# Performance work log

Measured on AMD Instinct MI355X. Metric: run time of the kernel, lower is better.

Reference implementation:

```python
import jax, jax.numpy as jnp
import numpy as np

C_IN, C_OUT, G = 64, 64, 32
D_MODEL = C_IN + 4 * G            # 192
DI = 2 * D_MODEL                  # d_inner = 384 (expand=2)
N_STATE = 16
DT_RANK = (D_MODEL + 15) // 16    # 12
K_DIR = 4
B, H, W = 2, 64, 64


def setup_inputs() -> dict:
    key = jax.random.key(0)
    ks = jax.random.split(key, 16)
    rn = lambda k, shp, s=0.02: jax.random.normal(k, shp, jnp.float32) * s
    inp = {"x": jax.random.normal(ks[0], (B, C_IN, H, W), jnp.float32)}
    chans = [C_IN, C_IN + G, C_IN + 2 * G, C_IN + 3 * G]
    for i, ci in enumerate(chans):
        inp[f"c{i+1}_w"] = rn(ks[1 + i], (G, ci, 3, 3))
        inp[f"c{i+1}_b"] = jnp.zeros((G,), jnp.float32)
    inp["c5_w"] = rn(ks[5], (C_OUT, D_MODEL, 3, 3))
    inp["c5_b"] = jnp.zeros((C_OUT,), jnp.float32)
    inp["ln1_g"] = jnp.ones((D_MODEL,), jnp.float32)
    inp["ln1_b"] = jnp.zeros((D_MODEL,), jnp.float32)
    inp["in_proj_w"] = rn(ks[6], (2 * DI, D_MODEL))
    inp["dw_w"] = rn(ks[7], (DI, 1, 3, 3))          # depthwise conv kernel
    inp["dw_b"] = jnp.zeros((DI,), jnp.float32)
    inp["x_proj_w"] = rn(ks[8], (K_DIR, DT_RANK + 2 * N_STATE, DI))
    inp["dt_w"] = rn(ks[9], (K_DIR, DI, DT_RANK), 0.1)
    inp["dt_b"] = jax.random.uniform(ks[10], (K_DIR, DI), jnp.float32, -4.0, -2.0)
    inp["A_logs"] = jnp.log(jnp.tile(jnp.arange(1, N_STATE + 1, dtype=jnp.float32), (K_DIR, DI, 1)))
    inp["Ds"] = jnp.ones((K_DIR, DI), jnp.float32)
    inp["out_norm_g"] = jnp.ones((DI,), jnp.float32)
    inp["out_norm_b"] = jnp.zeros((DI,), jnp.float32)
    inp["out_proj_w"] = rn(ks[11], (D_MODEL, DI))
    return inp


def conv2d(x, w, b, groups=1):
    y = jax.lax.conv_general_dilated(x, w, (1, 1), 'SAME',
                                     feature_group_count=groups,
                                     dimension_numbers=('NCHW', 'OIHW', 'NCHW'))
    return y + b[None, :, None, None]


def layer_norm(x, g, b, eps=1e-5):
    mu = jnp.mean(x, -1, keepdims=True)
    var = jnp.var(x, -1, keepdims=True)
    return (x - mu) * jax.lax.rsqrt(var + eps) * g + b


def selective_scan(u, delta, A, Bm, Cm, D):
    # u, delta: (B,K,Dm,L); Bm, Cm: (B,K,N,L); A: (K,Dm,N); D: (K,Dm)
    uL = jnp.moveaxis(u, -1, 0)
    dL = jnp.moveaxis(delta, -1, 0)
    BL = jnp.moveaxis(Bm, -1, 0)
    CL = jnp.moveaxis(Cm, -1, 0)
    h0 = jnp.zeros(u.shape[:3] + (A.shape[-1],), u.dtype)  # (B,K,Dm,N)

    def step(h, inp):
        u_l, d_l, B_l, C_l = inp
        dA = jnp.exp(d_l[..., None] * A)                              # (B,K,Dm,N)
        h = dA * h + (d_l * u_l)[..., None] * B_l[:, :, None, :]
        y = jnp.einsum('bkdn,bkn->bkd', h, C_l)
        return h, y

    _, ys = jax.lax.scan(step, h0, (uL, dL, BL, CL))
    y = jnp.moveaxis(ys, 0, -1)                                       # (B,K,Dm,L)
    return y + D[None, :, :, None] * u


def vss_block(x, ln1_g, ln1_b, in_proj_w, dw_w, dw_b, x_proj_w, dt_w, dt_b,
              A_logs, Ds, out_norm_g, out_norm_b, out_proj_w):
    Bn, C, Hh, Ww = x.shape
    L = Hh * Ww
    di = in_proj_w.shape[0] // 2
    nst = A_logs.shape[-1]
    dtr = dt_w.shape[-1]
    xi = jnp.transpose(x, (0, 2, 3, 1))                               # BHWC
    xn = layer_norm(xi, ln1_g, ln1_b)
    xz = xn @ in_proj_w.T                                             # (B,H,W,2*di)
    xp, z = jnp.split(xz, 2, -1)
    xc = jnp.transpose(xp, (0, 3, 1, 2))                              # (B,di,H,W)
    xc = jax.nn.silu(conv2d(xc, dw_w, dw_b, groups=di))
    xf = xc.reshape(Bn, di, L)
    xt = jnp.transpose(xc, (0, 1, 3, 2)).reshape(Bn, di, L)
    xs = jnp.stack([xf, xt, xf[..., ::-1], xt[..., ::-1]], 1)         # (B,4,di,L)
    x_dbl = jnp.einsum('bkdl,kcd->bkcl', xs, x_proj_w)
    dts = jnp.einsum('bkrl,kdr->bkdl', x_dbl[:, :, :dtr], dt_w)
    Bs = x_dbl[:, :, dtr:dtr + nst]
    Cs = x_dbl[:, :, dtr + nst:]
    delta = jax.nn.softplus(dts + dt_b[None, :, :, None])
    A = -jnp.exp(A_logs)
    oy = selective_scan(xs, delta, A, Bs, Cs, Ds)                     # (B,4,di,L)
    inv = oy[:, 2:4, :, ::-1]
    wh = jnp.transpose(oy[:, 1].reshape(Bn, di, Ww, Hh), (0, 1, 3, 2)).reshape(Bn, di, L)
    iwh = jnp.transpose(inv[:, 1].reshape(Bn, di, Ww, Hh), (0, 1, 3, 2)).reshape(Bn, di, L)
    y = oy[:, 0] + inv[:, 0] + wh + iwh
    y = jnp.transpose(y, (0, 2, 1)).reshape(Bn, Hh, Ww, di)
    y = layer_norm(y, out_norm_g, out_norm_b)
    y = y * jax.nn.silu(z)
    out = xi + y @ out_proj_w.T                                       # residual (VSSBlock)
    return jnp.transpose(out, (0, 3, 1, 2))


def reference(x, c1_w, c1_b, c2_w, c2_b, c3_w, c3_b, c4_w, c4_b, c5_w, c5_b,
              ln1_g, ln1_b, in_proj_w, dw_w, dw_b, x_proj_w, dt_w, dt_b,
              A_logs, Ds, out_norm_g, out_norm_b, out_proj_w):
    lrelu = lambda t: jax.nn.leaky_relu(t, 0.01)
    x1 = lrelu(conv2d(x, c1_w, c1_b))
    x2 = lrelu(conv2d(jnp.concatenate([x, x1], 1), c2_w, c2_b))
    x3 = lrelu(conv2d(jnp.concatenate([x, x1, x2], 1), c3_w, c3_b))
    x4 = lrelu(conv2d(jnp.concatenate([x, x1, x2, x3], 1), c4_w, c4_b))
    f = jnp.concatenate([x, x1, x2, x3, x4], 1)                       # (B,192,H,W)
    sa = vss_block(f, ln1_g, ln1_b, in_proj_w, dw_w, dw_b, x_proj_w, dt_w, dt_b,
                   A_logs, Ds, out_norm_g, out_norm_b, out_proj_w)
    return conv2d(sa, c5_w, c5_b)
```

## Files before the change

### kernel.cpp

```cpp
#include <hip/hip_runtime.h>
#include <hip/hip_bf16.h>
#include <math.h>

static constexpr int LEN = 4096;
static constexpr int HN  = 64;
static constexpr int WN  = 64;
static constexpr int NB  = 2;
static constexpr int DM  = 192;
static constexpr int DIM = 384;
static constexpr int NST = 16;
static constexpr int DTR = 12;
static constexpr int KD  = 4;
static constexpr int NC  = 64;
static constexpr int CHL = LEN / NC;

typedef __attribute__((ext_vector_type(8))) short bfrag;
typedef __attribute__((ext_vector_type(4))) float facc;

__device__ __forceinline__ unsigned short f2bf(float x) {
    unsigned int u = __float_as_uint(x);
    return (unsigned short)((u + 0x7FFFu + ((u >> 16) & 1u)) >> 16);
}

__device__ __forceinline__ int maprow(int k, int gl) {
    int g = (k & 2) ? (LEN - 1 - gl) : gl;
    return (k & 1) ? (((g & 63) << 6) | (g >> 6)) : g;
}

__global__ void k_wtr(const float* __restrict__ w, float* __restrict__ wt,
                      int cin, int cout, int n)
{
    int idx = blockIdx.x * 256 + threadIdx.x;
    if (idx >= n) return;
    int ci = idx % cin; int r = idx / cin;
    int co = r % cout; int t = r / cout;
    wt[idx] = w[((size_t)(co * cin + ci)) * 9 + t];
}

__global__ void k_wxp(const float* __restrict__ xpw, float* __restrict__ WX)
{
    int idx = blockIdx.x * 256 + threadIdx.x;
    if (idx >= 192 * DIM) return;
    int row = idx / DIM, d = idx - row * DIM;
    int k = row / 48, c = row - k * 48;
    WX[idx] = (c < 44) ? xpw[((size_t)(k * 44 + c)) * DIM + d] : 0.f;
}

__global__ void k_tr_in(const float* __restrict__ x, float* __restrict__ FN)
{
    __shared__ float t[64][65];
    int b = blockIdx.y, r = blockIdx.x;
    int tid = threadIdx.x;
#pragma unroll
    for (int i = 0; i < 16; ++i) {
        int idx = (i << 8) + tid;
        int c = idx >> 6, xc = idx & 63;
        t[c][xc] = x[((size_t)(b * 64 + c)) * LEN + r * WN + xc];
    }
    __syncthreads();
#pragma unroll
    for (int i = 0; i < 16; ++i) {
        int idx = (i << 8) + tid;
        int px = idx >> 6, c = idx & 63;
        FN[((size_t)(b * LEN + r * WN + px)) * DM + c] = t[c][px];
    }
}

__global__ void __launch_bounds__(256) k_convmf(
    const float* __restrict__ in, int cbuf, int cin, int cout,
    const float* __restrict__ wt2,
    float* __restrict__ part)
{
    __shared__ unsigned short Asb[66][40];
    __shared__ unsigned short Bsb[3][32][40];
    int zz = blockIdx.z;
    int b = zz / 3, s = zz % 3;
    int y0 = blockIdx.x;
    int n0 = blockIdx.y << 5;
    int tid = threadIdx.x;
    int wv = tid >> 6, lane = tid & 63;
    int mb  = (wv & 1) << 5;
    int nbw = (wv >> 1) << 4;
    int lr = lane & 15, lq = lane >> 4;
    int y = y0 + s - 1;
    bool yok = (unsigned)y < (unsigned)HN;
    const float* inb = in + ((size_t)b * LEN + (size_t)y * WN) * cbuf;

    facc acc0 = (facc){0,0,0,0}, acc1 = (facc){0,0,0,0};

    for (int ci0 = 0; ci0 < cin; ci0 += 32) {
#pragma unroll
        for (int it = 0; it < 3; ++it) {
            int fi = (it << 8) + tid;
            if (fi < 528) {
                int px = fi >> 3, c4 = (fi & 7) << 2;
                int xx = px - 1;
                float4 v = make_float4(0.f, 0.f, 0.f, 0.f);
                if (yok && (unsigned)xx < (unsigned)WN)
                    v = *(const float4*)(inb + (size_t)xx * cbuf + ci0 + c4);
                ushort4 u; u.x = f2bf(v.x); u.y = f2bf(v.y); u.z = f2bf(v.z); u.w = f2bf(v.w);
                *(ushort4*)(&Asb[px][c4]) = u;
            }
        }
#pragma unroll
        for (int it = 0; it < 3; ++it) {
            int fi = (it << 8) + tid;
            int dx = fi >> 8; int rem = fi & 255;
            int oc = rem >> 3, c4 = (rem & 7) << 2;
            int t = s * 3 + dx;
            float4 v = *(const float4*)(wt2 + ((size_t)(t * cout + n0 + oc)) * cin + ci0 + c4);
            ushort4 u; u.x = f2bf(v.x); u.y = f2bf(v.y); u.z = f2bf(v.z); u.w = f2bf(v.w);
            *(ushort4*)(&Bsb[dx][oc][c4]) = u;
        }
        __syncthreads();
#pragma unroll
        for (int dx = 0; dx < 3; ++dx) {
            bfrag a0 = *(const bfrag*)(&Asb[mb + lr + dx][lq * 8]);
            bfrag a1 = *(const bfrag*)(&Asb[mb + 16 + lr + dx][lq * 8]);
            bfrag b0 = *(const bfrag*)(&Bsb[dx][nbw + lr][lq * 8]);
            acc0 = __builtin_amdgcn_mfma_f32_16x16x32_bf16(a0, b0, acc0, 0, 0, 0);
            acc1 = __builtin_amdgcn_mfma_f32_16x16x32_bf16(a1, b0, acc1, 0, 0, 0);
        }
        __syncthreads();
    }
    float* pb = part + (((size_t)(s * NB + b) * LEN) + y0 * WN) * cout + n0 + nbw + lr;
#pragma unroll
    for (int r = 0; r < 4; ++r) {
        int px0 = mb + lq * 4 + r;
        pb[(size_t)px0 * cout] = acc0[r];
        pb[(size_t)(px0 + 16) * cout] = acc1[r];
    }
}

__global__ void k_ep_nhwc(const float* __restrict__ part, const float* __restrict__ bias,
                          float* __restrict__ FN, int co0, float slope)
{
    int idx = blockIdx.x * 256 + threadIdx.x;
    int co = idx & 31, px = idx >> 5;
    const size_t S = (size_t)NB * LEN * 32;
    float v = part[idx] + part[S + idx] + part[2 * S + idx] + bias[co];
    v = v > 0.f ? v : v * slope;
    FN[(size_t)px * DM + co0 + co] = v;
}

__global__ void k_ep_pl_tr(const float* __restrict__ part, const float* __restrict__ bias,
                           float* __restrict__ out)
{
    __shared__ float t[64][65];
    int b = blockIdx.y, l0 = blockIdx.x << 6;
    int tid = threadIdx.x;
    const size_t S = (size_t)NB * LEN * 64;
#pragma unroll
    for (int i = 0; i < 16; ++i) {
        int idx = (i << 8) + tid;
        int px = idx >> 6, oc = idx & 63;
        size_t o = ((size_t)b * LEN + l0 + px) * 64 + oc;
        t[px][oc] = part[o] + part[S + o] + part[2 * S + o] + bias[oc];
    }
    __syncthreads();
#pragma unroll
    for (int i = 0; i < 16; ++i) {
        int idx = (i << 8) + tid;
        int oc = idx >> 6, px = idx & 63;
        out[((size_t)(b * 64 + oc)) * LEN + l0 + px] = t[px][oc];
    }
}

__global__ void k_lnstat(const float* __restrict__ FN, float* __restrict__ MU,
                         float* __restrict__ RS)
{
    int lane = threadIdx.x & 63;
    int pix  = (blockIdx.x << 2) + (threadIdx.x >> 6);
    const float* fp = FN + (size_t)pix * DM;
    float v0 = fp[lane];
    float v1 = fp[lane + 64];
    float v2 = fp[lane + 128];
    float s = v0 + v1 + v2, ss = v0 * v0 + v1 * v1 + v2 * v2;
#pragma unroll
    for (int off = 1; off < 64; off <<= 1) { s += __shfl_xor(s, off); ss += __shfl_xor(ss, off); }
    if (lane == 0) {
        float mu = s * (1.f / 192.f);
        float var = ss * (1.f / 192.f) - mu * mu;
        MU[pix] = mu;
        RS[pix] = rsqrtf(var + 1e-5f);
    }
}

struct MfTile { facc a00, a01, a10, a11; int mb, nb, lr, lq; };

__device__ __forceinline__ MfTile mf_gemm_core(
    const float* __restrict__ A, int K, const float* __restrict__ Wt,
    int b, int l0, int n0, unsigned short (*Asb)[72], unsigned short (*Bsb)[72])
{
    int tid = threadIdx.x;
    MfTile t;
    t.a00 = (facc){0,0,0,0}; t.a01 = (facc){0,0,0,0};
    t.a10 = (facc){0,0,0,0}; t.a11 = (facc){0,0,0,0};
    int wv = tid >> 6, lane = tid & 63;
    t.mb = (wv & 1) << 5; t.nb = (wv >> 1) << 5;
    t.lr = lane & 15; t.lq = lane >> 4;

    for (int k0 = 0; k0 < K; k0 += 64) {
#pragma unroll
        for (int s = 0; s < 4; ++s) {
            int idx = (s << 8) + tid;
            int row = idx >> 4, c4 = (idx & 15) << 2;
            float4 av = *(const float4*)(A + ((size_t)b * LEN + l0 + row) * K + k0 + c4);
            ushort4 ua; ua.x = f2bf(av.x); ua.y = f2bf(av.y); ua.z = f2bf(av.z); ua.w = f2bf(av.w);
            *(ushort4*)(&Asb[row][c4]) = ua;
            float4 wvv = *(const float4*)(Wt + (size_t)(n0 + row) * K + k0 + c4);
            ushort4 ub; ub.x = f2bf(wvv.x); ub.y = f2bf(wvv.y); ub.z = f2bf(wvv.z); ub.w = f2bf(wvv.w);
            *(ushort4*)(&Bsb[row][c4]) = ub;
        }
        __syncthreads();
#pragma unroll
        for (int kk = 0; kk < 64; kk += 32) {
            bfrag a0 = *(const bfrag*)(&Asb[t.mb + t.lr][kk + t.lq * 8]);
            bfrag a1 = *(const bfrag*)(&Asb[t.mb + 16 + t.lr][kk + t.lq * 8]);
            bfrag b0 = *(const bfrag*)(&Bsb[t.nb + t.lr][kk + t.lq * 8]);
            bfrag b1 = *(const bfrag*)(&Bsb[t.nb + 16 + t.lr][kk + t.lq * 8]);
            t.a00 = __builtin_amdgcn_mfma_f32_16x16x32_bf16(a0, b0, t.a00, 0, 0, 0);
            t.a01 = __builtin_amdgcn_mfma_f32_16x16x32_bf16(a0, b1, t.a01, 0, 0, 0);
            t.a10 = __builtin_amdgcn_mfma_f32_16x16x32_bf16(a1, b0, t.a10, 0, 0, 0);
            t.a11 = __builtin_amdgcn_mfma_f32_16x16x32_bf16(a1, b1, t.a11, 0, 0, 0);
        }
        __syncthreads();
    }
    return t;
}

__device__ __forceinline__ void mf_store(
    facc v, float* __restrict__ Cp, const float* __restrict__ res,
    int b, int l0, int n0, int outC, int lr, int lq)
{
#pragma unroll
    for (int r = 0; r < 4; ++r) {
        int m = lq * 4 + r, n = lr;
        size_t o = ((size_t)b * LEN + l0 + m) * outC + n0 + n;
        float x = v[r];
        if (res) x += res[o];
        Cp[o] = x;
    }
}

__global__ void __launch_bounds__(256) k_gemm_mf(
    const float* __restrict__ A, int K, const float* __restrict__ Wt,
    const float* __restrict__ res, float* __restrict__ Cp, int outC)
{
    __shared__ unsigned short Asb[64][72];
    __shared__ unsigned short Bsb[64][72];
    int b = blockIdx.z, l0 = blockIdx.x << 6, n0 = blockIdx.y << 6;
    MfTile t = mf_gemm_core(A, K, Wt, b, l0, n0, Asb, Bsb);
    mf_store(t.a00, Cp, res, b, l0 + t.mb,      n0 + t.nb,      outC, t.lr, t.lq);
    mf_store(t.a01, Cp, res, b, l0 + t.mb,      n0 + t.nb + 16, outC, t.lr, t.lq);
    mf_store(t.a10, Cp, res, b, l0 + t.mb + 16, n0 + t.nb,      outC, t.lr, t.lq);
    mf_store(t.a11, Cp, res, b, l0 + t.mb + 16, n0 + t.nb + 16, outC, t.lr, t.lq);
}

__global__ void __launch_bounds__(256) k_gemm_ipmf(
    const float* __restrict__ A, const float* __restrict__ Wt,
    const float* __restrict__ g, const float* __restrict__ be,
    const float* __restrict__ MU, const float* __restrict__ RS,
    float* __restrict__ XPN, float* __restrict__ ZT)
{
    __shared__ unsigned short Asb[64][72];
    __shared__ unsigned short Bsb[64][72];
    int b = blockIdx.z, l0 = blockIdx.x << 6, n0 = blockIdx.y << 6;
    int tid = threadIdx.x;
    MfTile t;
    t.a00 = (facc){0,0,0,0}; t.a01 = (facc){0,0,0,0};
    t.a10 = (facc){0,0,0,0}; t.a11 = (facc){0,0,0,0};
    int wv = tid >> 6, lane = tid & 63;
    t.mb = (wv & 1) << 5; t.nb = (wv >> 1) << 5;
    t.lr = lane & 15; t.lq = lane >> 4;

    for (int k0 = 0; k0 < DM; k0 += 64) {
#pragma unroll
        for (int s = 0; s < 4; ++s) {
            int idx = (s << 8) + tid;
            int row = idx >> 4, c4 = (idx & 15) << 2;
            size_t pix = (size_t)b * LEN + l0 + row;
            float4 av = *(const float4*)(A + pix * DM + k0 + c4);
            float mu = MU[pix], rs = RS[pix];
            float4 gv = *(const float4*)(g + k0 + c4);
            float4 bv = *(const float4*)(be + k0 + c4);
            av.x = (av.x - mu) * rs * gv.x + bv.x;
            av.y = (av.y - mu) * rs * gv.y + bv.y;
            av.z = (av.z - mu) * rs * gv.z + bv.z;
            av.w = (av.w - mu) * rs * gv.w + bv.w;
            ushort4 ua; ua.x = f2bf(av.x); ua.y = f2bf(av.y); ua.z = f2bf(av.z); ua.w = f2bf(av.w);
            *(ushort4*)(&Asb[row][c4]) = ua;
            float4 wvv = *(const float4*)(Wt + (size_t)(n0 + row) * DM + k0 + c4);
            ushort4 ub; ub.x = f2bf(wvv.x); ub.y = f2bf(wvv.y); ub.z = f2bf(wvv.z); ub.w = f2bf(wvv.w);
            *(ushort4*)(&Bsb[row][c4]) = ub;
        }
        __syncthreads();
#pragma unroll
        for (int kk = 0; kk < 64; kk += 32) {
            bfrag a0 = *(const bfrag*)(&Asb[t.mb + t.lr][kk + t.lq * 8]);
            bfrag a1 = *(const bfrag*)(&Asb[t.mb + 16 + t.lr][kk + t.lq * 8]);
            bfrag b0 = *(const bfrag*)(&Bsb[t.nb + t.lr][kk + t.lq * 8]);
            bfrag b1 = *(const bfrag*)(&Bsb[t.nb + 16 + t.lr][kk + t.lq * 8]);
            t.a00 = __builtin_amdgcn_mfma_f32_16x16x32_bf16(a0, b0, t.a00, 0, 0, 0);
            t.a01 = __builtin_amdgcn_mfma_f32_16x16x32_bf16(a0, b1, t.a01, 0, 0, 0);
            t.a10 = __builtin_amdgcn_mfma_f32_16x16x32_bf16(a1, b0, t.a10, 0, 0, 0);
            t.a11 = __builtin_amdgcn_mfma_f32_16x16x32_bf16(a1, b1, t.a11, 0, 0, 0);
        }
        __syncthreads();
    }
    float* out = (blockIdx.y < 6) ? XPN : ZT;
    int nc = (blockIdx.y < 6) ? n0 : n0 - DIM;
    mf_store(t.a00, out, nullptr, b, l0 + t.mb,      nc + t.nb,      DIM, t.lr, t.lq);
    mf_store(t.a01, out, nullptr, b, l0 + t.mb,      nc + t.nb + 16, DIM, t.lr, t.lq);
    mf_store(t.a10, out, nullptr, b, l0 + t.mb + 16, nc + t.nb,      DIM, t.lr, t.lq);
    mf_store(t.a11, out, nullptr, b, l0 + t.mb + 16, nc + t.nb + 16, DIM, t.lr, t.lq);
}

__global__ void __launch_bounds__(256) k_dw(
    const float* __restrict__ xpn, const float* __restrict__ w,
    const float* __restrict__ bias, float* __restrict__ unh)
{
    int b = blockIdx.z, cg = blockIdx.y, r = blockIdx.x;
    int lane = threadIdx.x & 63, wv = threadIdx.x >> 6;
    int c = cg * 64 + lane;
    float wl[9];
#pragma unroll
    for (int t = 0; t < 9; ++t) wl[t] = w[c * 9 + t];
    float bv = bias[c];
    const float* base = xpn + (size_t)b * LEN * DIM + c;
    float* ob = unh + (size_t)b * LEN * DIM + c;
#pragma unroll 4
    for (int xi = 0; xi < 16; ++xi) {
        int x = wv * 16 + xi;
        float acc = bv;
#pragma unroll
        for (int dy = 0; dy < 3; ++dy) {
            int ry = r + dy - 1;
            if ((unsigned)ry >= (unsigned)HN) continue;
#pragma unroll
            for (int dx = 0; dx < 3; ++dx) {
                int xx = x + dx - 1;
                if ((unsigned)xx >= (unsigned)WN) continue;
                acc += base[(size_t)(ry * WN + xx) * DIM] * wl[dy * 3 + dx];
            }
        }
        acc = acc / (1.f + __expf(-acc));
        ob[(size_t)(r * WN + x) * DIM] = acc;
    }
}

__global__ void __launch_bounds__(384) k_delta(
    const float* __restrict__ CX, const float* __restrict__ dtw,
    const float* __restrict__ dtb, float* __restrict__ dlt)
{
    __shared__ float cs[16][12];
    int b = blockIdx.z, k = blockIdx.y;
    int lp0 = blockIdx.x << 4;
    int tid = threadIdx.x;
    if (tid < 192) {
        int p = tid / 12, r = tid - p * 12;
        cs[p][r] = CX[((size_t)(b * LEN) + lp0 + p) * 192 + k * 48 + r];
    }
    __syncthreads();
    float wt[DTR];
    const float* wp = dtw + ((size_t)(k * DIM) + tid) * DTR;
#pragma unroll
    for (int r = 0; r < DTR; ++r) wt[r] = wp[r];
    float bv = dtb[k * DIM + tid];
    float* dbase = dlt + (((size_t)(b * LEN) + lp0) * KD + k) * DIM + tid;
#pragma unroll
    for (int p = 0; p < 16; ++p) {
        float s = bv;
#pragma unroll
        for (int r = 0; r < DTR; ++r) s += cs[p][r] * wt[r];
        s = (s > 20.f) ? s : __logf(1.f + __expf(s));
        dbase[(size_t)p * KD * DIM] = s;
    }
}

__global__ void __launch_bounds__(384) k_scan_a(
    const float* __restrict__ unh, const float* __restrict__ CX,
    const float* __restrict__ alog, const float* __restrict__ dlt,
    float* __restrict__ hf, float* __restrict__ pA)
{
    __shared__ float bs[CHL * 16];
    int b = blockIdx.z, k = blockIdx.y, c = blockIdx.x;
    int d = threadIdx.x;
    for (int i = threadIdx.x; i < CHL * 16; i += 384) {
        int l = i >> 4, n = i & 15;
        int row = maprow(k, c * CHL + l);
        bs[i] = CX[((size_t)(b * LEN) + row) * 192 + k * 48 + 12 + n];
    }
    __syncthreads();

    float A[16], h[16];
    const float* ap = alog + ((size_t)(k * DIM + d)) * NST;
#pragma unroll
    for (int q = 0; q < 4; ++q) {
        float4 av = *(const float4*)(ap + q * 4);
        A[q * 4]     = -__expf(av.x); A[q * 4 + 1] = -__expf(av.y);
        A[q * 4 + 2] = -__expf(av.z); A[q * 4 + 3] = -__expf(av.w);
    }
    bool geo = true;
#pragma unroll
    for (int n = 1; n < 16; ++n)
        geo = geo && (fabsf(A[n] - (n + 1) * A[0]) <= 1e-4f * (n + 1) * fabsf(A[0]));
#pragma unroll
    for (int n = 0; n < 16; ++n) h[n] = 0.f;

    const float* ub = unh + (size_t)b * LEN * DIM + d;
    const float* db = dlt + ((size_t)(b * LEN) * KD + k) * DIM + d;
    size_t base = (((size_t)((b * KD + k) * NC + c)) * NST) * DIM + d;

    float dvA[4], uuA[4], dvB[4], uuB[4], dvC[4], uuC[4];
#pragma unroll
    for (int j = 0; j < 4; ++j) {
        int row = maprow(k, c * CHL + j);
        dvA[j] = db[(size_t)row * KD * DIM];
        uuA[j] = ub[(size_t)row * DIM];
    }
#pragma unroll
    for (int j = 0; j < 4; ++j) {
        int row = maprow(k, c * CHL + 4 + j);
        dvB[j] = db[(size_t)row * KD * DIM];
        uuB[j] = ub[(size_t)row * DIM];
    }

    if (geo) {
        float A0 = A[0];
        float p0 = 1.f;
        for (int l0 = 0; l0 < CHL; l0 += 4) {
            if (l0 + 8 < CHL) {
#pragma unroll
                for (int j = 0; j < 4; ++j) {
                    int row = maprow(k, c * CHL + l0 + 8 + j);
                    dvC[j] = db[(size_t)row * KD * DIM];
                    uuC[j] = ub[(size_t)row * DIM];
                }
            }
            __builtin_amdgcn_s_setprio(1);
#pragma unroll
            for (int j = 0; j < 4; ++j) {
                float du = dvA[j] * uuA[j];
                const float* bl = bs + (l0 + j) * 16;
                float qv = __expf(dvA[j] * A0);
                float pw = qv;
                h[0] = qv * h[0] + du * bl[0];
#pragma unroll
                for (int n = 1; n < 16; ++n) { pw *= qv; h[n] = pw * h[n] + du * bl[n]; }
                p0 *= qv;
            }
            __builtin_amdgcn_s_setprio(0);
#pragma unroll
            for (int j = 0; j < 4; ++j) { dvA[j] = dvB[j]; uuA[j] = uuB[j]; dvB[j] = dvC[j]; uuB[j] = uuC[j]; }
        }
        float pw = 1.f;
#pragma unroll
        for (int n = 0; n < 16; ++n) {
            pw *= p0;
            hf[base + (size_t)n * DIM] = h[n];
            pA[base + (size_t)n * DIM] = pw;
        }
    } else {
        float p[16];
#pragma unroll
        for (int n = 0; n < 16; ++n) p[n] = 1.f;
        for (int l0 = 0; l0 < CHL; l0 += 4) {
            if (l0 + 8 < CHL) {
#pragma unroll
                for (int j = 0; j < 4; ++j) {
                    int row = maprow(k, c * CHL + l0 + 8 + j);
                    dvC[j] = db[(size_t)row * KD * DIM];
                    uuC[j] = ub[(size_t)row * DIM];
                }
            }
#pragma unroll
            for (int j = 0; j < 4; ++j) {
                float du = dvA[j] * uuA[j];
                const float* bl = bs + (l0 + j) * 16;
#pragma unroll
                for (int n = 0; n < 16; ++n) {
                    float dA = __expf(dvA[j] * A[n]);
                    h[n] = dA * h[n] + du * bl[n];
                    p[n] *= dA;
                }
            }
#pragma unroll
            for (int j = 0; j < 4; ++j) { dvA[j] = dvB[j]; uuA[j] = uuB[j]; dvB[j] = dvC[j]; uuB[j] = uuC[j]; }
        }
#pragma unroll
        for (int n = 0; n < 16; ++n) {
            hf[base + (size_t)n * DIM] = h[n];
            pA[base + (size_t)n * DIM] = p[n];
        }
    }
}

__global__ void k_scan_b(float* __restrict__ hf, const float* __restrict__ pA)
{
    int s = blockIdx.x * 256 + threadIdx.x;
    int bk = s / (NST * DIM);
    int r  = s - bk * (NST * DIM);
    size_t base = (size_t)bk * NC * NST * DIM + r;
    const size_t cs = (size_t)NST * DIM;
    float car = 0.f;
#pragma unroll 8
    for (int c = 0; c < NC; ++c) {
        float hfc = hf[base + c * cs], pc = pA[base + c * cs];
        hf[base + c * cs] = car;
        car = pc * car + hfc;
    }
}

__global__ void __launch_bounds__(384) k_scan_c(
    const float* __restrict__ unh, const float* __restrict__ CX,
    const float* __restrict__ alog, const float* __restrict__ hf,
    float* __restrict__ dlt)
{
    __shared__ float bs[CHL * 32];
    int b = blockIdx.z, k = blockIdx.y, c = blockIdx.x;
    int d = threadIdx.x;
    for (int i = threadIdx.x; i < CHL * 32; i += 384) {
        int l = i >> 5, n = i & 31;
        int row = maprow(k, c * CHL + l);
        bs[i] = CX[((size_t)(b * LEN) + row) * 192 + k * 48 + 12 + n];
    }
    __syncthreads();

    float A[16], h[16];
    const float* ap = alog + ((size_t)(k * DIM + d)) * NST;
#pragma unroll
    for (int q = 0; q < 4; ++q) {
        float4 av = *(const float4*)(ap + q * 4);
        A[q * 4]     = -__expf(av.x); A[q * 4 + 1] = -__expf(av.y);
        A[q * 4 + 2] = -__expf(av.z); A[q * 4 + 3] = -__expf(av.w);
    }
    bool geo = true;
#pragma unroll
    for (int n = 1; n < 16; ++n)
        geo = geo && (fabsf(A[n] - (n + 1) * A[0]) <= 1e-4f * (n + 1) * fabsf(A[0]));
    size_t base = (((size_t)((b * KD + k) * NC + c)) * NST) * DIM + d;
#pragma unroll
    for (int n = 0; n < 16; ++n) h[n] = hf[base + (size_t)n * DIM];

    const float* ub = unh + (size_t)b * LEN * DIM + d;
    float* db = dlt + ((size_t)(b * LEN) * KD + k) * DIM + d;

    int rowsA[4], rowsB[4], rowsC[4];
    float dvA[4], uuA[4], dvB[4], uuB[4], dvC[4], uuC[4];
#pragma unroll
    for (int j = 0; j < 4; ++j) {
        rowsA[j] = maprow(k, c * CHL + j);
        dvA[j] = db[(size_t)rowsA[j] * KD * DIM];
        uuA[j] = ub[(size_t)rowsA[j] * DIM];
    }
#pragma unroll
    for (int j = 0; j < 4; ++j) {
        rowsB[j] = maprow(k, c * CHL + 4 + j);
        dvB[j] = db[(size_t)rowsB[j] * KD * DIM];
        uuB[j] = ub[(size_t)rowsB[j] * DIM];
    }

    if (geo) {
        float A0 = A[0];
        for (int l0 = 0; l0 < CHL; l0 += 4) {
            if (l0 + 8 < CHL) {
#pragma unroll
                for (int j = 0; j < 4; ++j) {
                    rowsC[j] = maprow(k, c * CHL + l0 + 8 + j);
                    dvC[j] = db[(size_t)rowsC[j] * KD * DIM];
                    uuC[j] = ub[(size_t)rowsC[j] * DIM];
                }
            }
            float ys[4];
            __builtin_amdgcn_s_setprio(1);
#pragma unroll
            for (int j = 0; j < 4; ++j) {
                const float* bl = bs + (l0 + j) * 32;
                float du = dvA[j] * uuA[j];
                float qv = __expf(dvA[j] * A0);
                float pw = qv;
                h[0] = qv * h[0] + du * bl[0];
                float y = h[0] * bl[16];
#pragma unroll
                for (int n = 1; n < 16; ++n) {
                    pw *= qv;
                    h[n] = pw * h[n] + du * bl[n];
                    y += h[n] * bl[16 + n];
                }
                ys[j] = y;
            }
            __builtin_amdgcn_s_setprio(0);
#pragma unroll
            for (int j = 0; j < 4; ++j) db[(size_t)rowsA[j] * KD * DIM] = ys[j];
#pragma unroll
            for (int j = 0; j < 4; ++j) {
                rowsA[j] = rowsB[j]; dvA[j] = dvB[j]; uuA[j] = uuB[j];
                rowsB[j] = rowsC[j]; dvB[j] = dvC[j]; uuB[j] = uuC[j];
            }
        }
    } else {
        for (int l0 = 0; l0 < CHL; l0 += 4) {
            if (l0 + 8 < CHL) {
#pragma unroll
                for (int j = 0; j < 4; ++j) {
                    rowsC[j] = maprow(k, c * CHL + l0 + 8 + j);
                    dvC[j] = db[(size_t)rowsC[j] * KD * DIM];
                    uuC[j] = ub[(size_t)rowsC[j] * DIM];
                }
            }
            float ys[4];
#pragma unroll
            for (int j = 0; j < 4; ++j) {
                const float* bl = bs + (l0 + j) * 32;
                float du = dvA[j] * uuA[j];
                float y = 0.f;
#pragma unroll
                for (int n = 0; n < 16; ++n) {
                    float dA = __expf(dvA[j] * A[n]);
                    h[n] = dA * h[n] + du * bl[n];
                    y += h[n] * bl[16 + n];
                }
                ys[j] = y;
            }
#pragma unroll
            for (int j = 0; j < 4; ++j) db[(size_t)rowsA[j] * KD * DIM] = ys[j];
#pragma unroll
            for (int j = 0; j < 4; ++j) {
                rowsA[j] = rowsB[j]; dvA[j] = dvB[j]; uuA[j] = uuB[j];
                rowsB[j] = rowsC[j]; dvB[j] = dvC[j]; uuB[j] = uuC[j];
            }
        }
    }
}

__global__ void k_merge(const float* __restrict__ y4, const float* __restrict__ unh,
                        const float* __restrict__ Ds, const float* __restrict__ ong,
                        const float* __restrict__ onb, const float* __restrict__ zt,
                        float* __restrict__ yg)
{
    int lane = threadIdx.x & 63;
    int pix = (blockIdx.x << 2) + (threadIdx.x >> 6);
    const float* yp = y4 + (size_t)pix * KD * DIM;
    const float* up = unh + (size_t)pix * DIM;
    float v[6]; float s = 0.f, ss = 0.f;
#pragma unroll
    for (int j = 0; j < 6; ++j) {
        int d = lane + (j << 6);
        float y = yp[d] + yp[DIM + d] + yp[2 * DIM + d] + yp[3 * DIM + d];
        float dsum = Ds[d] + Ds[DIM + d] + Ds[2 * DIM + d] + Ds[3 * DIM + d];
        y += dsum * up[d];
        v[j] = y; s += y; ss += y * y;
    }
#pragma unroll
    for (int off = 1; off < 64; off <<= 1) { s += __shfl_xor(s, off); ss += __shfl_xor(ss, off); }
    float mu = s * (1.f / 384.f);
    float var = ss * (1.f / 384.f) - mu * mu;
    float rstd = rsqrtf(var + 1e-5f);
    const float* zp = zt + (size_t)pix * DIM;
    float* op = yg + (size_t)pix * DIM;
#pragma unroll
    for (int j = 0; j < 6; ++j) {
        int d = lane + (j << 6);
        float zz = zp[d];
        float gate = zz / (1.f + __expf(-zz));
        op[d] = ((v[j] - mu) * rstd * ong[d] + onb[d]) * gate;
    }
}

extern "C" void kernel_launch(void* const* d_in, const int* in_sizes, int n_in,
                              void* d_out, int out_size, void* d_ws, size_t ws_size,
                              hipStream_t stream)
{
    const float* x    = (const float*)d_in[0];
    const float* c1w  = (const float*)d_in[1];  const float* c1b = (const float*)d_in[2];
    const float* c2w  = (const float*)d_in[3];  const float* c2b = (const float*)d_in[4];
    const float* c3w  = (const float*)d_in[5];  const float* c3b = (const float*)d_in[6];
    const float* c4w  = (const float*)d_in[7];  const float* c4b = (const float*)d_in[8];
    const float* c5w  = (const float*)d_in[9];  const float* c5b = (const float*)d_in[10];
    const float* ln1g = (const float*)d_in[11]; const float* ln1b= (const float*)d_in[12];
    const float* ipw  = (const float*)d_in[13];
    const float* dww  = (const float*)d_in[14]; const float* dwb = (const float*)d_in[15];
    const float* xpw  = (const float*)d_in[16];
    const float* dtw  = (const float*)d_in[17]; const float* dtb = (const float*)d_in[18];
    const float* alog = (const float*)d_in[19]; const float* dsv = (const float*)d_in[20];
    const float* ong  = (const float*)d_in[21]; const float* onb = (const float*)d_in[22];
    const float* opw  = (const float*)d_in[23];
    float* out = (float*)d_out;

    float* ws   = (float*)d_ws;
    float* FN   = ws;
    float* XN   = FN   + 1572864;
    float* XPN  = XN   + 1572864;
    float* ZT   = XPN  + 3145728;
    float* XCNH = ZT   + 3145728;
    float* DLT  = XCNH + 3145728;
    float* HF   = DLT  + 12582912;
    float* WT14 = HF   + 3145728;
    float* WT5  = WT14 + 129024;
    float* WX   = WT5  + 110592;
    float* MU   = WX   + 73728;
    float* RS   = MU   + 8192;
    float* PA = XPN;
    float* CX = XN;
    float* PART = XN;
    float* YN = DLT;

    k_wtr<<<dim3(72),  256, 0, stream>>>(c1w, WT14,          64, 32, 9 * 64 * 32);
    k_wtr<<<dim3(108), 256, 0, stream>>>(c2w, WT14 + 18432,  96, 32, 9 * 96 * 32);
    k_wtr<<<dim3(144), 256, 0, stream>>>(c3w, WT14 + 46080, 128, 32, 9 * 128 * 32);
    k_wtr<<<dim3(180), 256, 0, stream>>>(c4w, WT14 + 82944, 160, 32, 9 * 160 * 32);
    k_wtr<<<dim3(432), 256, 0, stream>>>(c5w, WT5,          192, 64, 9 * 192 * 64);
    k_wxp<<<dim3(288), 256, 0, stream>>>(xpw, WX);

    k_tr_in<<<dim3(HN, NB), 256, 0, stream>>>(x, FN);
    k_convmf<<<dim3(64, 1, NB * 3), 256, 0, stream>>>(FN, DM, 64, 32, WT14, PART);
    k_ep_nhwc<<<dim3(1024), 256, 0, stream>>>(PART, c1b, FN, 64, 0.01f);
    k_convmf<<<dim3(64, 1, NB * 3), 256, 0, stream>>>(FN, DM, 96, 32, WT14 + 18432, PART);
    k_ep_nhwc<<<dim3(1024), 256, 0, stream>>>(PART, c2b, FN, 96, 0.01f);
    k_convmf<<<dim3(64, 1, NB * 3), 256, 0, stream>>>(FN, DM, 128, 32, WT14 + 46080, PART);
    k_ep_nhwc<<<dim3(1024), 256, 0, stream>>>(PART, c3b, FN, 128, 0.01f);
    k_convmf<<<dim3(64, 1, NB * 3), 256, 0, stream>>>(FN, DM, 160, 32, WT14 + 82944, PART);
    k_ep_nhwc<<<dim3(1024), 256, 0, stream>>>(PART, c4b, FN, 160, 0.01f);

    k_lnstat<<<dim3(NB * LEN / 4), 256, 0, stream>>>(FN, MU, RS);
    k_gemm_ipmf<<<dim3(LEN / 64, 12, NB), 256, 0, stream>>>(FN, ipw, ln1g, ln1b, MU, RS, XPN, ZT);
    k_dw<<<dim3(HN, DIM / 64, NB), 256, 0, stream>>>(XPN, dww, dwb, XCNH);
    k_gemm_mf<<<dim3(LEN / 64, 3, NB), 256, 0, stream>>>(XCNH, DIM, WX, nullptr, CX, 192);
    k_delta<<<dim3(LEN / 16, KD, NB), 384, 0, stream>>>(CX, dtw, dtb, DLT);
    k_scan_a<<<dim3(NC, KD, NB), 384, 0, stream>>>(XCNH, CX, alog, DLT, HF, PA);
    k_scan_b<<<dim3(NB * KD * NST * DIM / 256), 256, 0, stream>>>(HF, PA);
    k_scan_c<<<dim3(NC, KD, NB), 384, 0, stream>>>(XCNH, CX, alog, HF, DLT);
    k_merge<<<dim3(NB * LEN / 4), 256, 0, stream>>>(DLT, XCNH, dsv, ong, onb, ZT, XCNH);
    k_gemm_mf<<<dim3(LEN / 64, 3, NB), 256, 0, stream>>>(XCNH, DIM, opw, FN, YN, DM);

    k_convmf<<<dim3(64, 2, NB * 3), 256, 0, stream>>>(YN, DM, 192, 64, WT5, PART);
    k_ep_pl_tr<<<dim3(64, NB), 256, 0, stream>>>(PART, c5b, out);
}
```

Measured before the change: 297.5 us.

## Split scan state dimension across two half-wavefronts to double thread parallelism

Both chunked selective-scan kernels now launch 768 threads per block, with each channel's 16 state entries split between two half-wavefronts of 8. The geometric power chain is shortened by computing powers up to p8 and scaling the upper half by p8. The output y is combined with a cross-half shuffle, and the geometric-check flag is shared the same way. This cuts the serial per-thread work and register pressure so more waves can hide latency. In exchange, each lane loads delta and u redundantly, shuffles are added, and half the lanes sit idle on the store.

```diff
diff --git a/kernel.cpp b/kernel.cpp
--- a/kernel.cpp
+++ b/kernel.cpp
@@ -378,35 +378,44 @@
     }
 }
 
-__global__ void __launch_bounds__(384) k_scan_a(
+__global__ void __launch_bounds__(768) k_scan_a(
     const float* __restrict__ unh, const float* __restrict__ CX,
     const float* __restrict__ alog, const float* __restrict__ dlt,
     float* __restrict__ hf, float* __restrict__ pA)
 {
     __shared__ float bs[CHL * 16];
     int b = blockIdx.z, k = blockIdx.y, c = blockIdx.x;
-    int d = threadIdx.x;
-    for (int i = threadIdx.x; i < CHL * 16; i += 384) {
+    int tid = threadIdx.x;
+    int lane = tid & 63;
+    int d = ((tid >> 6) << 5) + (lane & 31);
+    int half = lane >> 5;
+    int nh = half << 3;
+
+    for (int i = tid; i < CHL * 16; i += 768) {
         int l = i >> 4, n = i & 15;
         int row = maprow(k, c * CHL + l);
         bs[i] = CX[((size_t)(b * LEN) + row) * 192 + k * 48 + 12 + n];
     }
     __syncthreads();
 
-    float A[16], h[16];
+    float A[8], h[8];
     const float* ap = alog + ((size_t)(k * DIM + d)) * NST;
-#pragma unroll
-    for (int q = 0; q < 4; ++q) {
-        float4 av = *(const float4*)(ap + q * 4);
+    float A0 = -__expf(ap[0]);
+#pragma unroll
+    for (int q = 0; q < 2; ++q) {
+        float4 av = *(const float4*)(ap + nh + q * 4);
         A[q * 4]     = -__expf(av.x); A[q * 4 + 1] = -__expf(av.y);
         A[q * 4 + 2] = -__expf(av.z); A[q * 4 + 3] = -__expf(av.w);
     }
     bool geo = true;
 #pragma unroll
-    for (int n = 1; n < 16; ++n)
-        geo = geo && (fabsf(A[n] - (n + 1) * A[0]) <= 1e-4f * (n + 1) * fabsf(A[0]));
-#pragma unroll
-    for (int n = 0; n < 16; ++n) h[n] = 0.f;
+    for (int i = 0; i < 8; ++i) {
+        int n = nh + i;
+        geo = geo && (fabsf(A[i] - (n + 1) * A0) <= 1e-4f * (n + 1) * fabsf(A0));
+    }
+    geo = geo && (bool)__shfl_xor((int)geo, 32);
+#pragma unroll
+    for (int i = 0; i < 8; ++i) h[i] = 0.f;
 
     const float* ub = unh + (size_t)b * LEN * DIM + d;
     const float* db = dlt + ((size_t)(b * LEN) * KD + k) * DIM + d;
@@ -427,7 +436,6 @@
     }
 
     if (geo) {
-        float A0 = A[0];
         float p0 = 1.f;
         for (int l0 = 0; l0 < CHL; l0 += 4) {
             if (l0 + 8 < CHL) {
@@ -442,29 +450,38 @@
 #pragma unroll
             for (int j = 0; j < 4; ++j) {
                 float du = dvA[j] * uuA[j];
-                const float* bl = bs + (l0 + j) * 16;
+                const float* bl = bs + (l0 + j) * 16 + nh;
                 float qv = __expf(dvA[j] * A0);
-                float pw = qv;
-                h[0] = qv * h[0] + du * bl[0];
-#pragma unroll
-                for (int n = 1; n < 16; ++n) { pw *= qv; h[n] = pw * h[n] + du * bl[n]; }
+                float p2 = qv * qv, p3 = p2 * qv, p4 = p2 * p2;
+                float p5 = p4 * qv, p6 = p4 * p2, p7 = p4 * p3, p8 = p4 * p4;
+                float m = half ? p8 : 1.f;
+                h[0] = (qv * m) * h[0] + du * bl[0];
+                h[1] = (p2 * m) * h[1] + du * bl[1];
+                h[2] = (p3 * m) * h[2] + du * bl[2];
+                h[3] = (p4 * m) * h[3] + du * bl[3];
+                h[4] = (p5 * m) * h[4] + du * bl[4];
+                h[5] = (p6 * m) * h[5] + du * bl[5];
+                h[6] = (p7 * m) * h[6] + du * bl[6];
+                h[7] = (p8 * m) * h[7] + du * bl[7];
                 p0 *= qv;
             }
             __builtin_amdgcn_s_setprio(0);
 #pragma unroll
             for (int j = 0; j < 4; ++j) { dvA[j] = dvB[j]; uuA[j] = uuB[j]; dvB[j] = dvC[j]; uuB[j] = uuC[j]; }
         }
-        float pw = 1.f;
-#pragma unroll
-        for (int n = 0; n < 16; ++n) {
-            pw *= p0;
-            hf[base + (size_t)n * DIM] = h[n];
-            pA[base + (size_t)n * DIM] = pw;
+        float q2 = p0 * p0, q3 = q2 * p0, q4 = q2 * q2;
+        float q5 = q4 * p0, q6 = q4 * q2, q7 = q4 * q3, q8 = q4 * q4;
+        float m0 = half ? q8 : 1.f;
+        float Pw[8] = {p0 * m0, q2 * m0, q3 * m0, q4 * m0, q5 * m0, q6 * m0, q7 * m0, q8 * m0};
+#pragma unroll
+        for (int i = 0; i < 8; ++i) {
+            hf[base + (size_t)(nh + i) * DIM] = h[i];
+            pA[base + (size_t)(nh + i) * DIM] = Pw[i];
         }
     } else {
-        float p[16];
-#pragma unroll
-        for (int n = 0; n < 16; ++n) p[n] = 1.f;
+        float p[8];
+#pragma unroll
+        for (int i = 0; i < 8; ++i) p[i] = 1.f;
         for (int l0 = 0; l0 < CHL; l0 += 4) {
             if (l0 + 8 < CHL) {
 #pragma unroll
@@ -477,21 +494,21 @@
 #pragma unroll
             for (int j = 0; j < 4; ++j) {
                 float du = dvA[j] * uuA[j];
-                const float* bl = bs + (l0 + j) * 16;
-#pragma unroll
-                for (int n = 0; n < 16; ++n) {
-                    float dA = __expf(dvA[j] * A[n]);
-                    h[n] = dA * h[n] + du * bl[n];
-                    p[n] *= dA;
+                const float* bl = bs + (l0 + j) * 16 + nh;
+#pragma unroll
+                for (int i = 0; i < 8; ++i) {
+                    float dA = __expf(dvA[j] * A[i]);
+                    h[i] = dA * h[i] + du * bl[i];
+                    p[i] *= dA;
                 }
             }
 #pragma unroll
             for (int j = 0; j < 4; ++j) { dvA[j] = dvB[j]; uuA[j] = uuB[j]; dvB[j] = dvC[j]; uuB[j] = uuC[j]; }
         }
 #pragma unroll
-        for (int n = 0; n < 16; ++n) {
-            hf[base + (size_t)n * DIM] = h[n];
-            pA[base + (size_t)n * DIM] = p[n];
+        for (int i = 0; i < 8; ++i) {
+            hf[base + (size_t)(nh + i) * DIM] = h[i];
+            pA[base + (size_t)(nh + i) * DIM] = p[i];
         }
     }
 }
@@ -512,36 +529,45 @@
     }
 }
 
-__global__ void __launch_bounds__(384) k_scan_c(
+__global__ void __launch_bounds__(768) k_scan_c(
     const float* __restrict__ unh, const float* __restrict__ CX,
     const float* __restrict__ alog, const float* __restrict__ hf,
     float* __restrict__ dlt)
 {
     __shared__ float bs[CHL * 32];
     int b = blockIdx.z, k = blockIdx.y, c = blockIdx.x;
-    int d = threadIdx.x;
-    for (int i = threadIdx.x; i < CHL * 32; i += 384) {
+    int tid = threadIdx.x;
+    int lane = tid & 63;
+    int d = ((tid >> 6) << 5) + (lane & 31);
+    int half = lane >> 5;
+    int nh = half << 3;
+
+    for (int i = tid; i < CHL * 32; i += 768) {
         int l = i >> 5, n = i & 31;
         int row = maprow(k, c * CHL + l);
         bs[i] = CX[((size_t)(b * LEN) + row) * 192 + k * 48 + 12 + n];
     }
     __syncthreads();
 
-    float A[16], h[16];
+    float A[8], h[8];
     const float* ap = alog + ((size_t)(k * DIM + d)) * NST;
-#pragma unroll
-    for (int q = 0; q < 4; ++q) {
-        float4 av = *(const float4*)(ap + q * 4);
+    float A0 = -__expf(ap[0]);
+#pragma unroll
+    for (int q = 0; q < 2; ++q) {
+        float4 av = *(const float4*)(ap + nh + q * 4);
         A[q * 4]     = -__expf(av.x); A[q * 4 + 1] = -__expf(av.y);
         A[q * 4 + 2] = -__expf(av.z); A[q * 4 + 3] = -__expf(av.w);
     }
     bool geo = true;
 #pragma unroll
-    for (int n = 1; n < 16; ++n)
-        geo = geo && (fabsf(A[n] - (n + 1) * A[0]) <= 1e-4f * (n + 1) * fabsf(A[0]));
+    for (int i = 0; i < 8; ++i) {
+        int n = nh + i;
+        geo = geo && (fabsf(A[i] - (n + 1) * A0) <= 1e-4f * (n + 1) * fabsf(A0));
+    }
+    geo = geo && (bool)__shfl_xor((int)geo, 32);
     size_t base = (((size_t)((b * KD + k) * NC + c)) * NST) * DIM + d;
 #pragma unroll
-    for (int n = 0; n < 16; ++n) h[n] = hf[base + (size_t)n * DIM];
+    for (int i = 0; i < 8; ++i) h[i] = hf[base + (size_t)(nh + i) * DIM];
 
     const float* ub = unh + (size_t)b * LEN * DIM + d;
     float* db = dlt + ((size_t)(b * LEN) * KD + k) * DIM + d;
@@ -562,7 +588,6 @@
     }
 
     if (geo) {
-        float A0 = A[0];
         for (int l0 = 0; l0 < CHL; l0 += 4) {
             if (l0 + 8 < CHL) {
 #pragma unroll
@@ -576,23 +601,30 @@
             __builtin_amdgcn_s_setprio(1);
 #pragma unroll
             for (int j = 0; j < 4; ++j) {
-                const float* bl = bs + (l0 + j) * 32;
+                const float* bl = bs + (l0 + j) * 32 + nh;
                 float du = dvA[j] * uuA[j];
                 float qv = __expf(dvA[j] * A0);
-                float pw = qv;
-                h[0] = qv * h[0] + du * bl[0];
-                float y = h[0] * bl[16];
-#pragma unroll
-                for (int n = 1; n < 16; ++n) {
-                    pw *= qv;
-                    h[n] = pw * h[n] + du * bl[n];
-                    y += h[n] * bl[16 + n];
-                }
+                float p2 = qv * qv, p3 = p2 * qv, p4 = p2 * p2;
+                float p5 = p4 * qv, p6 = p4 * p2, p7 = p4 * p3, p8 = p4 * p4;
+                float m = half ? p8 : 1.f;
+                float y = 0.f;
+                h[0] = (qv * m) * h[0] + du * bl[0]; y += h[0] * bl[16];
+                h[1] = (p2 * m) * h[1] + du * bl[1]; y += h[1] * bl[17];
+                h[2] = (p3 * m) * h[2] + du * bl[2]; y += h[2] * bl[18];
+                h[3] = (p4 * m) * h[3] + du * bl[3]; y += h[3] * bl[19];
+                h[4] = (p5 * m) * h[4] + du * bl[4]; y += h[4] * bl[20];
+                h[5] = (p6 * m) * h[5] + du * bl[5]; y += h[5] * bl[21];
+                h[6] = (p7 * m) * h[6] + du * bl[6]; y += h[6] * bl[22];
+                h[7] = (p8 * m) * h[7] + du * bl[7]; y += h[7] * bl[23];
                 ys[j] = y;
             }
             __builtin_amdgcn_s_setprio(0);
 #pragma unroll
-            for (int j = 0; j < 4; ++j) db[(size_t)rowsA[j] * KD * DIM] = ys[j];
+            for (int j = 0; j < 4; ++j) ys[j] += __shfl_xor(ys[j], 32);
+            if (!half) {
+#pragma unroll
+                for (int j = 0; j < 4; ++j) db[(size_t)rowsA[j] * KD * DIM] = ys[j];
+            }
 #pragma unroll
             for (int j = 0; j < 4; ++j) {
                 rowsA[j] = rowsB[j]; dvA[j] = dvB[j]; uuA[j] = uuB[j];
@@ -612,19 +644,23 @@
             float ys[4];
 #pragma unroll
             for (int j = 0; j < 4; ++j) {
-                const float* bl = bs + (l0 + j) * 32;
+                const float* bl = bs + (l0 + j) * 32 + nh;
                 float du = dvA[j] * uuA[j];
                 float y = 0.f;
 #pragma unroll
-                for (int n = 0; n < 16; ++n) {
-                    float dA = __expf(dvA[j] * A[n]);
-                    h[n] = dA * h[n] + du * bl[n];
-                    y += h[n] * bl[16 + n];
+                for (int i = 0; i < 8; ++i) {
+                    float dA = __expf(dvA[j] * A[i]);
+                    h[i] = dA * h[i] + du * bl[i];
+                    y += h[i] * bl[16 + i];
                 }
                 ys[j] = y;
             }
 #pragma unroll
-            for (int j = 0; j < 4; ++j) db[(size_t)rowsA[j] * KD * DIM] = ys[j];
+            for (int j = 0; j < 4; ++j) ys[j] += __shfl_xor(ys[j], 32);
+            if (!half) {
+#pragma unroll
+                for (int j = 0; j < 4; ++j) db[(size_t)rowsA[j] * KD * DIM] = ys[j];
+            }
 #pragma unroll
             for (int j = 0; j < 4; ++j) {
                 rowsA[j] = rowsB[j]; dvA[j] = dvB[j]; uuA[j] = uuB[j];
@@ -728,9 +764,9 @@
     k_dw<<<dim3(HN, DIM / 64, NB), 256, 0, stream>>>(XPN, dww, dwb, XCNH);
     k_gemm_mf<<<dim3(LEN / 64, 3, NB), 256, 0, stream>>>(XCNH, DIM, WX, nullptr, CX, 192);
     k_delta<<<dim3(LEN / 16, KD, NB), 384, 0, stream>>>(CX, dtw, dtb, DLT);
-    k_scan_a<<<dim3(NC, KD, NB), 384, 0, stream>>>(XCNH, CX, alog, DLT, HF, PA);
+    k_scan_a<<<dim3(NC, KD, NB), 768, 0, stream>>>(XCNH, CX, alog, DLT, HF, PA);
     k_scan_b<<<dim3(NB * KD * NST * DIM / 256), 256, 0, stream>>>(HF, PA);
-    k_scan_c<<<dim3(NC, KD, NB), 384, 0, stream>>>(XCNH, CX, alog, HF, DLT);
+    k_scan_c<<<dim3(NC, KD, NB), 768, 0, stream>>>(XCNH, CX, alog, HF, DLT);
     k_merge<<<dim3(NB * LEN / 4), 256, 0, stream>>>(DLT, XCNH, dsv, ong, onb, ZT, XCNH);
     k_gemm_mf<<<dim3(LEN / 64, 3, NB), 256, 0, stream>>>(XCNH, DIM, opw, FN, YN, DM);
 
```

Result: no change. 303.1 us (+1.9%).
